# Performance work log

Hardware: AMD Instinct MI355X
Metric: run time of the kernel (lower is better)

The kernel has to match this reference:

```python
import jax, jax.numpy as jnp
import numpy as np

N, E, D_IN, D_OUT, H = 50000, 800000, 128, 128, 4
D_H = D_OUT // H


def setup_inputs() -> dict:
    key = jax.random.key(0)
    ks = jax.random.split(key, 6)
    x = jax.random.normal(ks[0], (N, D_IN), dtype=jnp.float32)
    edge_index = jax.random.randint(ks[1], (2, E), 0, N, dtype=jnp.int64)
    # parameters (xavier-ish scaling)
    W = jax.random.normal(ks[2], (D_IN, D_OUT), dtype=jnp.float32) * (1.0 / np.sqrt(D_IN))
    attn_vec = jax.random.normal(ks[3], (H, 2 * D_H), dtype=jnp.float32) * (1.0 / np.sqrt(2 * D_H))
    out_w = jax.random.normal(ks[4], (D_OUT, D_OUT), dtype=jnp.float32) * (1.0 / np.sqrt(D_OUT))
    out_b = jax.random.normal(ks[5], (D_OUT,), dtype=jnp.float32) * 0.01
    return {"x": x, "edge_index": edge_index, "W": W, "attn_vec": attn_vec,
            "out_w": out_w, "out_b": out_b}


def reference(x, edge_index, W, attn_vec, out_w, out_b):
    n = x.shape[0]
    Wx = (x @ W).reshape(n, H, D_H)                      # [N,H,d_h]
    src, dst = edge_index[0], edge_index[1]
    h_src = Wx[src]                                      # [E,H,d_h]
    h_dst = Wx[dst]                                      # [E,H,d_h]
    a_i = attn_vec[:, :D_H]                              # [H,d_h]
    a_j = attn_vec[:, D_H:]                              # [H,d_h]
    e = jnp.einsum('ehd,hd->eh', h_src, a_i) + jnp.einsum('ehd,hd->eh', h_dst, a_j)
    e = jax.nn.leaky_relu(e, negative_slope=0.2)         # [E,H]
    # segment softmax over incoming edges per destination node
    e_max = jax.ops.segment_max(e, dst, num_segments=n)  # [N,H]
    exp_e = jnp.exp(e - e_max[dst])                      # [E,H]
    exp_sum = jax.ops.segment_sum(exp_e, dst, num_segments=n)  # [N,H]
    alpha = exp_e / (exp_sum[dst] + 1e-16)               # [E,H]
    # weighted scatter-add aggregation
    agg = jax.ops.segment_sum(alpha[:, :, None] * h_src, dst, num_segments=n)  # [N,H,d_h]
    out = agg.reshape(n, D_OUT) @ out_w + out_b
    return jax.nn.elu(out)
```

## Files before the change

kernel.cpp:

```cpp
#include <hip/hip_runtime.h>
#include <math.h>


typedef __attribute__((ext_vector_type(8))) short short8;
typedef __attribute__((ext_vector_type(4))) float f32x4;

#define BIN_VPT 16

__device__ __forceinline__ float lrelu(float v) { return v >= 0.f ? v : 0.2f * v; }

__device__ __forceinline__ unsigned short f2bf(float f) {
  unsigned int u = __float_as_uint(f);
  u += 0x7FFFu + ((u >> 16) & 1u);
  return (unsigned short)(u >> 16);
}
__device__ __forceinline__ float bflo(unsigned int w) { return __uint_as_float(w << 16); }
__device__ __forceinline__ float bfhi(unsigned int w) { return __uint_as_float(w & 0xFFFF0000u); }

__device__ __forceinline__ int blk_excl_scan(int v, int* ws) {
  const int t = threadIdx.x, lane = t & 63, wv = t >> 6;
  int incl = v;
#pragma unroll
  for (int m = 1; m < 64; m <<= 1) {
    int x = __shfl_up(incl, m, 64);
    if (lane >= m) incl += x;
  }
  if (lane == 63) ws[wv] = incl;
  __syncthreads();
  int woff = 0;
  for (int p = 0; p < wv; ++p) woff += ws[p];
  return woff + incl - v;
}

__global__ void k_setup(const float* __restrict__ W, const float* __restrict__ ow,
                        unsigned short* __restrict__ wf, unsigned short* __restrict__ owf,
                        int* __restrict__ gcnt, int* __restrict__ gcur) {
  const int t = blockIdx.x * 256 + threadIdx.x;
  if (blockIdx.x == 0) gcnt[threadIdx.x] = 0;
  if (blockIdx.x == 1) gcur[threadIdx.x] = 0;
  const int which = t >> 11;
  const int tt = t & 2047;
  const float* M = which ? ow : W;
  unsigned short* F = which ? owf : wf;
  const int lane = tt & 63;
  const int nt = (tt >> 6) & 7;
  const int ks = tt >> 9;
  const int k0 = ks * 32 + (lane >> 4) * 8;
  const int col = nt * 16 + (lane & 15);
  short8 v;
#pragma unroll
  for (int j = 0; j < 8; ++j) v[j] = (short)f2bf(M[(k0 + j) * 128 + col]);
  *(short8*)(F + (size_t)tt * 8) = v;
}

__global__ void k_gemm1b(const float* __restrict__ x, const unsigned short* __restrict__ wf,
                         const float* __restrict__ attn, unsigned int* __restrict__ Wxb,
                         float* __restrict__ s_i, float* __restrict__ s_j, int n,
                         const int* __restrict__ dst, int* __restrict__ gcnt, int E,
                         int gemmBlocks) {
  __shared__ int lc[256];
  if (blockIdx.x >= gemmBlocks) {
    const int bb = blockIdx.x - gemmBlocks;
    lc[threadIdx.x] = 0;
    __syncthreads();
    const int base = bb * (256 * BIN_VPT);
#pragma unroll
    for (int j = 0; j < BIN_VPT; ++j) {
      int e = base + j * 256 + threadIdx.x;
      if (e < E) atomicAdd(&lc[((unsigned int)dst[e]) >> 8], 1);
    }
    __syncthreads();
    int c = lc[threadIdx.x];
    if (c) atomicAdd(&gcnt[threadIdx.x], c);
    return;
  }

  const int lane = threadIdx.x & 63;
  const int gw = blockIdx.x * (blockDim.x >> 6) + (threadIdx.x >> 6);
  const int r0 = gw * 16;
  if (r0 >= n) return;
  const int g = lane >> 4, c = lane & 15;

  f32x4 acc[8];
#pragma unroll
  for (int nt = 0; nt < 8; ++nt) acc[nt] = (f32x4){0.f, 0.f, 0.f, 0.f};

  const int arow = min(r0 + c, n - 1);
#pragma unroll
  for (int ks = 0; ks < 4; ++ks) {
    const float* xr = x + (size_t)arow * 128 + ks * 32 + g * 8;
    float4 v0 = *(const float4*)xr;
    float4 v1 = *(const float4*)(xr + 4);
    short8 af;
    af[0] = (short)f2bf(v0.x); af[1] = (short)f2bf(v0.y);
    af[2] = (short)f2bf(v0.z); af[3] = (short)f2bf(v0.w);
    af[4] = (short)f2bf(v1.x); af[5] = (short)f2bf(v1.y);
    af[6] = (short)f2bf(v1.z); af[7] = (short)f2bf(v1.w);
#pragma unroll
    for (int nt = 0; nt < 8; ++nt) {
      short8 bf = *(const short8*)(wf + ((size_t)(ks * 8 + nt) * 64 + lane) * 8);
      acc[nt] = __builtin_amdgcn_mfma_f32_16x16x32_bf16(af, bf, acc[nt], 0, 0, 0);
    }
  }

  const int odd = c & 1;
#pragma unroll
  for (int r = 0; r < 4; ++r) {
    const int row = r0 + g * 4 + r;
    if (row >= n) continue;
    unsigned int* dp = Wxb + (size_t)row * 64;
#pragma unroll
    for (int ntp = 0; ntp < 4; ++ntp) {
      float ve = acc[ntp][r], vo = acc[ntp + 4][r];
      float vex = __shfl_xor(ve, 1, 64);
      float vox = __shfl_xor(vo, 1, 64);
      unsigned int lo = odd ? f2bf(vox) : f2bf(ve);
      unsigned int hi = odd ? f2bf(vo) : f2bf(vex);
      const int nt = odd ? ntp + 4 : ntp;
      dp[nt * 8 + (c >> 1)] = lo | (hi << 16);
    }
  }

  float aiv[8], ajv[8];
#pragma unroll
  for (int nt = 0; nt < 8; ++nt) {
    const int hh = nt >> 1, ch = (nt & 1) * 16 + c;
    aiv[nt] = attn[hh * 64 + ch];
    ajv[nt] = attn[hh * 64 + 32 + ch];
  }
#pragma unroll
  for (int r = 0; r < 4; ++r) {
    float pih[4], pjh[4];
#pragma unroll
    for (int h = 0; h < 4; ++h) {
      pih[h] = acc[2 * h][r] * aiv[2 * h] + acc[2 * h + 1][r] * aiv[2 * h + 1];
      pjh[h] = acc[2 * h][r] * ajv[2 * h] + acc[2 * h + 1][r] * ajv[2 * h + 1];
    }
#pragma unroll
    for (int m = 1; m < 16; m <<= 1) {
#pragma unroll
      for (int h = 0; h < 4; ++h) {
        pih[h] += __shfl_xor(pih[h], m, 64);
        pjh[h] += __shfl_xor(pjh[h], m, 64);
      }
    }
    const int row = r0 + g * 4 + r;
    if (c == 0 && row < n) {
#pragma unroll
      for (int h = 0; h < 4; ++h) {
        s_i[(size_t)row * 4 + h] = pih[h];
        s_j[(size_t)row * 4 + h] = pjh[h];
      }
    }
  }
}

__global__ void k_bin1(const int* __restrict__ edges, const int* __restrict__ gcnt,
                       int* __restrict__ gcur, unsigned int* __restrict__ tmp, int E) {
  __shared__ int ws[4];
  __shared__ int bst_s[256];
  __shared__ int lcnt[256];
  __shared__ int lbase[256];
  const int t = threadIdx.x;
  const int excl = blk_excl_scan(gcnt[t], ws);
  bst_s[t] = excl;
  lcnt[t] = 0;
  __syncthreads();
  const int base = blockIdx.x * (256 * BIN_VPT);
  unsigned int pv[BIN_VPT];
  int rk[BIN_VPT];
#pragma unroll
  for (int j = 0; j < BIN_VPT; ++j) {
    int e = base + j * 256 + t;
    if (e < E) {
      unsigned int s = (unsigned int)edges[e];
      unsigned int d = (unsigned int)edges[E + e];
      pv[j] = s | (d << 16);
      rk[j] = atomicAdd(&lcnt[d >> 8], 1);
    } else {
      pv[j] = 0u;
      rk[j] = -1;
    }
  }
  __syncthreads();
  const int c = lcnt[t];
  lbase[t] = bst_s[t] + (c ? atomicAdd(&gcur[t], c) : 0);
  __syncthreads();
#pragma unroll
  for (int j = 0; j < BIN_VPT; ++j) {
    if (rk[j] >= 0) {
      const int b = pv[j] >> 24;
      tmp[lbase[b] + rk[j]] = pv[j];
    }
  }
}

__global__ void k_bin2(const unsigned int* __restrict__ tmp, const int* __restrict__ gcnt,
                       int* __restrict__ csr, int* __restrict__ offs,
                       int* __restrict__ cnts, int n) {
  __shared__ int ws[4];
  __shared__ int bst_s[256];
  __shared__ int nc[256];
  const int b = blockIdx.x;
  const int t = threadIdx.x;
  bst_s[t] = blk_excl_scan(gcnt[t], ws);
  nc[t] = 0;
  __syncthreads();
  const int base = bst_s[b], cnt = gcnt[b];
  for (int i = t; i < cnt; i += 256)
    atomicAdd(&nc[(tmp[base + i] >> 16) & 255], 1);
  __syncthreads();
  const int node = b * 256 + t;
  const int c = nc[t];
  if (node < n) cnts[node] = c;
  __syncthreads();
  const int excl = blk_excl_scan(c, ws);
  if (node < n) offs[node] = base + excl;
  __syncthreads();
  nc[t] = excl;
  __syncthreads();
  for (int i = t; i < cnt; i += 256) {
    unsigned int v = tmp[base + i];
    int pos = atomicAdd(&nc[(v >> 16) & 255], 1);
    csr[base + pos] = (int)(v & 0xFFFFu);
  }
}

#define AGG_WPB 4
__global__ void k_agg(const unsigned int* __restrict__ Wxb, const float* __restrict__ s_i,
                      const float* __restrict__ s_j, const int* __restrict__ offs,
                      const int* __restrict__ cnts, const int* __restrict__ csr_src,
                      unsigned int* __restrict__ aggb, int n) {
  __shared__ int   lsrc[AGG_WPB][64];
  __shared__ float lp[AGG_WPB][64][4];
  const int lane = threadIdx.x & 63;
  const int wv = threadIdx.x >> 6;
  const int nd = blockIdx.x * AGG_WPB + wv;
  if (nd >= n) return;
  const int base = offs[nd];
  const int deg = cnts[nd];
  const float4 sj = *(const float4*)(s_j + (size_t)nd * 4);
  const int h = lane >> 4;

  float4 smp = make_float4(0.f, 0.f, 0.f, 0.f);
  float2 acc = make_float2(0.f, 0.f);
  for (int c0 = 0; c0 < deg; c0 += 64) {
    const int m = min(64, deg - c0);
    if (lane < m) {
      int src = csr_src[base + c0 + lane];
      float4 si = *(const float4*)(s_i + (size_t)src * 4);
      float4 p;
      p.x = __expf(lrelu(si.x + sj.x));
      p.y = __expf(lrelu(si.y + sj.y));
      p.z = __expf(lrelu(si.z + sj.z));
      p.w = __expf(lrelu(si.w + sj.w));
      smp.x += p.x; smp.y += p.y; smp.z += p.z; smp.w += p.w;
      lsrc[wv][lane] = src;
      *(float4*)&lp[wv][lane][0] = p;
    }
    asm volatile("s_waitcnt lgkmcnt(0)" ::: "memory");
    int k = 0;
    for (; k + 8 <= m; k += 8) {
      int s0 = lsrc[wv][k + 0], s1 = lsrc[wv][k + 1];
      int s2 = lsrc[wv][k + 2], s3 = lsrc[wv][k + 3];
      int s4 = lsrc[wv][k + 4], s5 = lsrc[wv][k + 5];
      int s6 = lsrc[wv][k + 6], s7 = lsrc[wv][k + 7];
      float p0 = lp[wv][k + 0][h], p1 = lp[wv][k + 1][h];
      float p2 = lp[wv][k + 2][h], p3 = lp[wv][k + 3][h];
      float p4 = lp[wv][k + 4][h], p5 = lp[wv][k + 5][h];
      float p6 = lp[wv][k + 6][h], p7 = lp[wv][k + 7][h];
      unsigned int w0 = Wxb[(size_t)s0 * 64 + lane];
      unsigned int w1 = Wxb[(size_t)s1 * 64 + lane];
      unsigned int w2 = Wxb[(size_t)s2 * 64 + lane];
      unsigned int w3 = Wxb[(size_t)s3 * 64 + lane];
      unsigned int w4 = Wxb[(size_t)s4 * 64 + lane];
      unsigned int w5 = Wxb[(size_t)s5 * 64 + lane];
      unsigned int w6 = Wxb[(size_t)s6 * 64 + lane];
      unsigned int w7 = Wxb[(size_t)s7 * 64 + lane];
      acc.x += p0 * bflo(w0); acc.y += p0 * bfhi(w0);
      acc.x += p1 * bflo(w1); acc.y += p1 * bfhi(w1);
      acc.x += p2 * bflo(w2); acc.y += p2 * bfhi(w2);
      acc.x += p3 * bflo(w3); acc.y += p3 * bfhi(w3);
      acc.x += p4 * bflo(w4); acc.y += p4 * bfhi(w4);
      acc.x += p5 * bflo(w5); acc.y += p5 * bfhi(w5);
      acc.x += p6 * bflo(w6); acc.y += p6 * bfhi(w6);
      acc.x += p7 * bflo(w7); acc.y += p7 * bfhi(w7);
    }
    for (; k + 4 <= m; k += 4) {
      int s0 = lsrc[wv][k + 0], s1 = lsrc[wv][k + 1];
      int s2 = lsrc[wv][k + 2], s3 = lsrc[wv][k + 3];
      float p0 = lp[wv][k + 0][h], p1 = lp[wv][k + 1][h];
      float p2 = lp[wv][k + 2][h], p3 = lp[wv][k + 3][h];
      unsigned int w0 = Wxb[(size_t)s0 * 64 + lane];
      unsigned int w1 = Wxb[(size_t)s1 * 64 + lane];
      unsigned int w2 = Wxb[(size_t)s2 * 64 + lane];
      unsigned int w3 = Wxb[(size_t)s3 * 64 + lane];
      acc.x += p0 * bflo(w0); acc.y += p0 * bfhi(w0);
      acc.x += p1 * bflo(w1); acc.y += p1 * bfhi(w1);
      acc.x += p2 * bflo(w2); acc.y += p2 * bfhi(w2);
      acc.x += p3 * bflo(w3); acc.y += p3 * bfhi(w3);
    }
    for (; k < m; ++k) {
      int s = lsrc[wv][k];
      float pv = lp[wv][k][h];
      unsigned int w = Wxb[(size_t)s * 64 + lane];
      acc.x += pv * bflo(w); acc.y += pv * bfhi(w);
    }
  }
#pragma unroll
  for (int m = 1; m < 64; m <<= 1) {
    smp.x += __shfl_xor(smp.x, m, 64);
    smp.y += __shfl_xor(smp.y, m, 64);
    smp.z += __shfl_xor(smp.z, m, 64);
    smp.w += __shfl_xor(smp.w, m, 64);
  }
  float sh = (h & 2) ? ((h & 1) ? smp.w : smp.z) : ((h & 1) ? smp.y : smp.x);
  const float inv = 1.f / (sh + 1e-16f);
  unsigned int lo = f2bf(acc.x * inv), hi = f2bf(acc.y * inv);
  aggb[(size_t)nd * 64 + lane] = lo | (hi << 16);
}

__global__ void k_gemm2(const unsigned int* __restrict__ aggb,
                        const unsigned short* __restrict__ owf,
                        const float* __restrict__ ob, float* __restrict__ out, int n) {
  const int lane = threadIdx.x & 63;
  const int gw = blockIdx.x * (blockDim.x >> 6) + (threadIdx.x >> 6);
  const int r0 = gw * 16;
  if (r0 >= n) return;
  const int g = lane >> 4, c = lane & 15;

  f32x4 acc[8];
#pragma unroll
  for (int nt = 0; nt < 8; ++nt) acc[nt] = (f32x4){0.f, 0.f, 0.f, 0.f};

  const int arow = min(r0 + c, n - 1);
#pragma unroll
  for (int ks = 0; ks < 4; ++ks) {
    const unsigned int* ar = aggb + (size_t)arow * 64 + ks * 16 + g * 4;
    uint4 av = *(const uint4*)ar;
    short8 af;
    af[0] = (short)(av.x & 0xFFFF); af[1] = (short)(av.x >> 16);
    af[2] = (short)(av.y & 0xFFFF); af[3] = (short)(av.y >> 16);
    af[4] = (short)(av.z & 0xFFFF); af[5] = (short)(av.z >> 16);
    af[6] = (short)(av.w & 0xFFFF); af[7] = (short)(av.w >> 16);
#pragma unroll
    for (int nt = 0; nt < 8; ++nt) {
      short8 bf = *(const short8*)(owf + ((size_t)(ks * 8 + nt) * 64 + lane) * 8);
      acc[nt] = __builtin_amdgcn_mfma_f32_16x16x32_bf16(af, bf, acc[nt], 0, 0, 0);
    }
  }

#pragma unroll
  for (int r = 0; r < 4; ++r) {
    const int row = r0 + g * 4 + r;
    if (row >= n) continue;
    float* dst = out + (size_t)row * 128;
#pragma unroll
    for (int nt = 0; nt < 8; ++nt) {
      float v = acc[nt][r] + ob[nt * 16 + c];
      v = v > 0.f ? v : expm1f(v);
      dst[nt * 16 + c] = v;
    }
  }
}

extern "C" void kernel_launch(void* const* d_in, const int* in_sizes, int n_in,
                              void* d_out, int out_size, void* d_ws, size_t ws_size,
                              hipStream_t stream) {
  const float* x    = (const float*)d_in[0];
  const int*   edges = (const int*)d_in[1];
  const float* W    = (const float*)d_in[2];
  const float* attn = (const float*)d_in[3];
  const float* ow   = (const float*)d_in[4];
  const float* ob   = (const float*)d_in[5];
  const int n = in_sizes[0] / 128;
  const int E = in_sizes[1] / 2;
  float* out = (float*)d_out;

  char* wp = (char*)d_ws;
  auto alloc = [&](size_t bytes) {
    char* p = wp;
    wp += (bytes + 255) & ~(size_t)255;
    return p;
  };
  unsigned short* wf  = (unsigned short*)alloc(2048 * 8 * 2);
  unsigned short* owf = (unsigned short*)alloc(2048 * 8 * 2);
  unsigned int*   Wxb = (unsigned int*)alloc((size_t)n * 64 * 4);
  unsigned int*   agb = (unsigned int*)alloc((size_t)n * 64 * 4);
  float* s_i    = (float*)alloc((size_t)n * 4 * 4);
  float* s_j    = (float*)alloc((size_t)n * 4 * 4);
  int*   gcnt   = (int*)alloc(256 * 4);
  int*   gcur   = (int*)alloc(256 * 4);
  int*   offs   = (int*)alloc((size_t)n * 4);
  int*   cnts   = (int*)alloc((size_t)n * 4);
  unsigned int* tmp = (unsigned int*)alloc((size_t)E * 4);
  int*   csr    = (int*)alloc((size_t)E * 4);

  dim3 blk(256);
  const int NB = (n + 255) / 256;
  const int EB = (E + 256 * BIN_VPT - 1) / (256 * BIN_VPT);
  const int strips = (n + 15) / 16;
  const int gemmBlocks = (strips + 3) / 4;

  k_setup<<<16, blk, 0, stream>>>(W, ow, wf, owf, gcnt, gcur);
  k_gemm1b<<<gemmBlocks + EB, blk, 0, stream>>>(x, wf, attn, Wxb, s_i, s_j, n,
                                                edges + E, gcnt, E, gemmBlocks);
  k_bin1<<<EB, blk, 0, stream>>>(edges, gcnt, gcur, tmp, E);
  k_bin2<<<NB, blk, 0, stream>>>(tmp, gcnt, csr, offs, cnts, n);
  k_agg<<<(n + AGG_WPB - 1) / AGG_WPB, blk, 0, stream>>>(Wxb, s_i, s_j, offs, cnts, csr, agb, n);
  k_gemm2<<<gemmBlocks, blk, 0, stream>>>(agb, owf, ob, out, n);
}
```

Baseline: 106.7 us.

## Fuse aggregation with output GEMM and use packed bf16 conversion instruction

Merges the aggregation kernel and the second GEMM into one kernel. Each 1024-thread block aggregates 16 destination nodes, one per wave, and stages the bf16 rows in LDS. Eight waves then run the MFMA output projection with bias and ELU. This drops the aggb global round trip and one kernel launch, and replaces software bf16 rounding with the hardware v_cvt_pk_bf16_f32 instruction. In exchange, the large blocks and a block-wide barrier make all 16 waves wait for the highest-degree node, and only half the waves do the GEMM.

```diff
diff --git a/kernel.cpp b/kernel.cpp
--- a/kernel.cpp
+++ b/kernel.cpp
@@ -13,6 +13,11 @@
   unsigned int u = __float_as_uint(f);
   u += 0x7FFFu + ((u >> 16) & 1u);
   return (unsigned short)(u >> 16);
+}
+__device__ __forceinline__ unsigned int cvt_pk_bf16(float lo, float hi) {
+  unsigned int r;
+  asm("v_cvt_pk_bf16_f32 %0, %1, %2" : "=v"(r) : "v"(lo), "v"(hi));
+  return r;
 }
 __device__ __forceinline__ float bflo(unsigned int w) { return __uint_as_float(w << 16); }
 __device__ __forceinline__ float bfhi(unsigned int w) { return __uint_as_float(w & 0xFFFF0000u); }
@@ -91,11 +96,12 @@
     const float* xr = x + (size_t)arow * 128 + ks * 32 + g * 8;
     float4 v0 = *(const float4*)xr;
     float4 v1 = *(const float4*)(xr + 4);
-    short8 af;
-    af[0] = (short)f2bf(v0.x); af[1] = (short)f2bf(v0.y);
-    af[2] = (short)f2bf(v0.z); af[3] = (short)f2bf(v0.w);
-    af[4] = (short)f2bf(v1.x); af[5] = (short)f2bf(v1.y);
-    af[6] = (short)f2bf(v1.z); af[7] = (short)f2bf(v1.w);
+    uint4 au;
+    au.x = cvt_pk_bf16(v0.x, v0.y);
+    au.y = cvt_pk_bf16(v0.z, v0.w);
+    au.z = cvt_pk_bf16(v1.x, v1.y);
+    au.w = cvt_pk_bf16(v1.z, v1.w);
+    short8 af = __builtin_bit_cast(short8, au);
 #pragma unroll
     for (int nt = 0; nt < 8; ++nt) {
       short8 bf = *(const short8*)(wf + ((size_t)(ks * 8 + nt) * 64 + lane) * 8);
@@ -114,10 +120,8 @@
       float ve = acc[ntp][r], vo = acc[ntp + 4][r];
       float vex = __shfl_xor(ve, 1, 64);
       float vox = __shfl_xor(vo, 1, 64);
-      unsigned int lo = odd ? f2bf(vox) : f2bf(ve);
-      unsigned int hi = odd ? f2bf(vo) : f2bf(vex);
       const int nt = odd ? ntp + 4 : ntp;
-      dp[nt * 8 + (c >> 1)] = lo | (hi << 16);
+      dp[nt * 8 + (c >> 1)] = cvt_pk_bf16(odd ? vox : ve, odd ? vo : vex);
     }
   }
 
@@ -226,21 +230,27 @@
   }
 }
 
-#define AGG_WPB 4
-__global__ void k_agg(const unsigned int* __restrict__ Wxb, const float* __restrict__ s_i,
-                      const float* __restrict__ s_j, const int* __restrict__ offs,
-                      const int* __restrict__ cnts, const int* __restrict__ csr_src,
-                      unsigned int* __restrict__ aggb, int n) {
-  __shared__ int   lsrc[AGG_WPB][64];
-  __shared__ float lp[AGG_WPB][64][4];
+__global__ void k_aggm(const unsigned int* __restrict__ Wxb, const float* __restrict__ s_i,
+                       const float* __restrict__ s_j, const int* __restrict__ offs,
+                       const int* __restrict__ cnts, const int* __restrict__ csr_src,
+                       const unsigned short* __restrict__ owf, const float* __restrict__ ob,
+                       float* __restrict__ out, int n) {
+  __shared__ unsigned int aTile[16][65];
+  __shared__ int   lsrc[16][64];
+  __shared__ float lp[16][64][4];
   const int lane = threadIdx.x & 63;
   const int wv = threadIdx.x >> 6;
-  const int nd = blockIdx.x * AGG_WPB + wv;
-  if (nd >= n) return;
-  const int base = offs[nd];
-  const int deg = cnts[nd];
-  const float4 sj = *(const float4*)(s_j + (size_t)nd * 4);
+  const int nd0 = blockIdx.x * 16;
+  const int nd = nd0 + wv;
   const int h = lane >> 4;
+
+  int base = 0, deg = 0;
+  float4 sj = make_float4(0.f, 0.f, 0.f, 0.f);
+  if (nd < n) {
+    base = offs[nd];
+    deg = cnts[nd];
+    sj = *(const float4*)(s_j + (size_t)nd * 4);
+  }
 
   float4 smp = make_float4(0.f, 0.f, 0.f, 0.f);
   float2 acc = make_float2(0.f, 0.f);
@@ -316,50 +326,28 @@
   }
   float sh = (h & 2) ? ((h & 1) ? smp.w : smp.z) : ((h & 1) ? smp.y : smp.x);
   const float inv = 1.f / (sh + 1e-16f);
-  unsigned int lo = f2bf(acc.x * inv), hi = f2bf(acc.y * inv);
-  aggb[(size_t)nd * 64 + lane] = lo | (hi << 16);
-}
-
-__global__ void k_gemm2(const unsigned int* __restrict__ aggb,
-                        const unsigned short* __restrict__ owf,
-                        const float* __restrict__ ob, float* __restrict__ out, int n) {
-  const int lane = threadIdx.x & 63;
-  const int gw = blockIdx.x * (blockDim.x >> 6) + (threadIdx.x >> 6);
-  const int r0 = gw * 16;
-  if (r0 >= n) return;
-  const int g = lane >> 4, c = lane & 15;
-
-  f32x4 acc[8];
-#pragma unroll
-  for (int nt = 0; nt < 8; ++nt) acc[nt] = (f32x4){0.f, 0.f, 0.f, 0.f};
-
-  const int arow = min(r0 + c, n - 1);
-#pragma unroll
-  for (int ks = 0; ks < 4; ++ks) {
-    const unsigned int* ar = aggb + (size_t)arow * 64 + ks * 16 + g * 4;
-    uint4 av = *(const uint4*)ar;
-    short8 af;
-    af[0] = (short)(av.x & 0xFFFF); af[1] = (short)(av.x >> 16);
-    af[2] = (short)(av.y & 0xFFFF); af[3] = (short)(av.y >> 16);
-    af[4] = (short)(av.z & 0xFFFF); af[5] = (short)(av.z >> 16);
-    af[6] = (short)(av.w & 0xFFFF); af[7] = (short)(av.w >> 16);
-#pragma unroll
-    for (int nt = 0; nt < 8; ++nt) {
+  aTile[wv][lane] = cvt_pk_bf16(acc.x * inv, acc.y * inv);
+  __syncthreads();
+
+  if (wv < 8) {
+    const int g = lane >> 4, c = lane & 15;
+    const int nt = wv;
+    f32x4 o = (f32x4){0.f, 0.f, 0.f, 0.f};
+#pragma unroll
+    for (int ks = 0; ks < 4; ++ks) {
+      uint4 au = *(const uint4*)&aTile[c][ks * 16 + g * 4];
+      short8 af = __builtin_bit_cast(short8, au);
       short8 bf = *(const short8*)(owf + ((size_t)(ks * 8 + nt) * 64 + lane) * 8);
-      acc[nt] = __builtin_amdgcn_mfma_f32_16x16x32_bf16(af, bf, acc[nt], 0, 0, 0);
-    }
-  }
-
-#pragma unroll
-  for (int r = 0; r < 4; ++r) {
-    const int row = r0 + g * 4 + r;
-    if (row >= n) continue;
-    float* dst = out + (size_t)row * 128;
-#pragma unroll
-    for (int nt = 0; nt < 8; ++nt) {
-      float v = acc[nt][r] + ob[nt * 16 + c];
-      v = v > 0.f ? v : expm1f(v);
-      dst[nt * 16 + c] = v;
+      o = __builtin_amdgcn_mfma_f32_16x16x32_bf16(af, bf, o, 0, 0, 0);
+    }
+#pragma unroll
+    for (int r = 0; r < 4; ++r) {
+      const int row = nd0 + g * 4 + r;
+      if (row < n) {
+        float v = o[r] + ob[nt * 16 + c];
+        v = v > 0.f ? v : expm1f(v);
+        out[(size_t)row * 128 + nt * 16 + c] = v;
+      }
     }
   }
 }
@@ -386,7 +374,6 @@
   unsigned short* wf  = (unsigned short*)alloc(2048 * 8 * 2);
   unsigned short* owf = (unsigned short*)alloc(2048 * 8 * 2);
   unsigned int*   Wxb = (unsigned int*)alloc((size_t)n * 64 * 4);
-  unsigned int*   agb = (unsigned int*)alloc((size_t)n * 64 * 4);
   float* s_i    = (float*)alloc((size_t)n * 4 * 4);
   float* s_j    = (float*)alloc((size_t)n * 4 * 4);
   int*   gcnt   = (int*)alloc(256 * 4);
@@ -407,6 +394,6 @@
                                                 edges + E, gcnt, E, gemmBlocks);
   k_bin1<<<EB, blk, 0, stream>>>(edges, gcnt, gcur, tmp, E);
   k_bin2<<<NB, blk, 0, stream>>>(tmp, gcnt, csr, offs, cnts, n);
-  k_agg<<<(n + AGG_WPB - 1) / AGG_WPB, blk, 0, stream>>>(Wxb, s_i, s_j, offs, cnts, csr, agb, n);
-  k_gemm2<<<gemmBlocks, blk, 0, stream>>>(agb, owf, ob, out, n);
-}
+  k_aggm<<<(n + 15) / 16, dim3(1024), 0, stream>>>(Wxb, s_i, s_j, offs, cnts, csr,
+                                                   owf, ob, out, n);
+}
```

Result: faster. 104.1 us (-2.5%).
